# Kernel tuning notes

Hardware: AMD Instinct MI355X
Metric: run time of the kernel (lower is better)

The kernel has to match this reference:

```python
import jax, jax.numpy as jnp
import numpy as np

VNUMS = [4248, 4258, 5327, 3721, 5404, 2818]
B, C, H, W = 12, 64, 192, 192
DV, HID, BOX = 128, 256, 32


def _roi_patches(imgs, pros, imgbatch, box_len=BOX):
    # torchvision roi_align (aligned=False, sampling_ratio -> 1 sample per 1x1 bin):
    # bilinear sample at bin centers x1 + (j+0.5), y1 + (i+0.5)
    ar = jnp.arange(box_len, dtype=pros.dtype) + 0.5
    xs = pros[:, 0:1] - box_len / 2.0 + ar  # [G, box]
    ys = pros[:, 1:2] - box_len / 2.0 + ar  # [G, box]
    img_g = imgs[imgbatch]  # [G, C, H, W]

    def sample_one(img_chw, ys1, xs1):
        yy, xx = jnp.meshgrid(ys1, xs1, indexing="ij")  # [box, box]
        def per_c(ch):
            return jax.scipy.ndimage.map_coordinates(ch, [yy, xx], order=1, mode="nearest")
        return jax.vmap(per_c)(img_chw)  # [C, box, box]

    return jax.vmap(sample_one)(img_g, ys, xs)  # [G, C, box, box]


def setup_inputs() -> dict:
    key = jax.random.key(0)
    ks = jax.random.split(key, 6)
    G = 2 * B
    gtypes = np.array([(g // 2) % 6 if g % 2 == 0 else ((g // 2) + 3) % 6 for g in range(G)], dtype=np.int64)
    vnums_g = np.array([VNUMS[t] for t in gtypes])
    off = np.concatenate([[0], np.cumsum(vnums_g)])
    Nv = int(off[-1])  # 103104
    gar_of_vert = np.repeat(np.arange(G), vnums_g)
    idxs = []
    for t in range(6):
        gl = np.nonzero(gtypes == t)[0]
        idxs.append(np.concatenate([off[g] + np.arange(VNUMS[t]) for g in gl]).astype(np.int32))
    Din = DV + C
    pros = jax.random.uniform(ks[1], (G, 2), jnp.float32) * (H - 2.0 * BOX) + BOX
    inp = {
        "imgs": jax.random.normal(ks[0], (B, C, H, W), jnp.float32),
        "pros": pros,
        "x_verts": jax.random.normal(ks[2], (Nv, DV), jnp.float32),
        "W1": jax.random.normal(ks[3], (6, Din, HID), jnp.float32) / np.sqrt(Din).astype(np.float32),
        "W2": jax.random.normal(ks[4], (6, HID, HID), jnp.float32) / np.sqrt(HID).astype(np.float32),
        "W3": jax.random.normal(ks[5], (6, HID, 3), jnp.float32) / np.sqrt(HID).astype(np.float32),
        "imgbatch": jnp.asarray(np.arange(G) // 2, jnp.int32),
        "gar_of_vert": jnp.asarray(gar_of_vert, jnp.int32),
    }
    for t in range(6):
        inp[f"idx_t{t}"] = jnp.asarray(idxs[t])
    return inp


def reference(imgs, pros, x_verts, W1, W2, W3, imgbatch, gar_of_vert,
              idx_t0, idx_t1, idx_t2, idx_t3, idx_t4, idx_t5):
    # 1) roi_align patch extraction + pooled per-garment image feature
    patches = _roi_patches(imgs, pros, imgbatch)        # [G, C, 32, 32]
    garf = patches.mean(axis=(2, 3))                     # [G, C]
    # 2) per-vertex feature = [vertex feat | garment image feat]
    feat = jnp.concatenate([x_verts, garf[gar_of_vert]], axis=-1)  # [Nv, DV+C]
    # 3) MoE-style dispatch per garment type -> per-type expert MLP -> scatter-combine
    out = jnp.zeros((x_verts.shape[0], 3), feat.dtype)
    for t, idx in enumerate([idx_t0, idx_t1, idx_t2, idx_t3, idx_t4, idx_t5]):
        ft = feat[idx]                                   # gather (dispatch)
        h = jax.nn.relu(ft @ W1[t])
        h = jax.nn.relu(h @ W2[t])
        out = out.at[idx].set(h @ W3[t])                 # scatter (combine)
    return out
```

## Files before the change

kernel.cpp:

```cpp
#include <hip/hip_runtime.h>

typedef __attribute__((ext_vector_type(8))) short short8;
typedef __attribute__((ext_vector_type(4))) float float4_;

__device__ __forceinline__ unsigned short f2bf(float f) {
    unsigned u = __float_as_uint(f);
    u += 0x7FFFu + ((u >> 16) & 1u);
    return (unsigned short)(u >> 16);
}

__global__ void prep_weights(const float* __restrict__ W1,
                             const float* __restrict__ W2,
                             const float* __restrict__ W3,
                             unsigned short* __restrict__ w1t,
                             unsigned short* __restrict__ w2t,
                             unsigned short* __restrict__ w3t) {
    int id = blockIdx.x * 256 + threadIdx.x;
    if (id < 294912) {
        int t = id / 49152, r = id % 49152;
        int n = r / 192, k = r % 192;
        w1t[id] = f2bf(W1[(size_t)t * 49152 + k * 256 + n]);
    } else if (id < 688128) {
        int i2 = id - 294912;
        int t = i2 / 65536, r = i2 % 65536;
        int n = r / 256, k = r % 256;
        w2t[i2] = f2bf(W2[(size_t)t * 65536 + k * 256 + n]);
    } else if (id < 712704) {
        int i3 = id - 688128;
        int t = i3 / 4096, r = i3 % 4096;
        int n = r / 256, k = r % 256;
        w3t[i3] = (n < 3) ? f2bf(W3[(size_t)t * 768 + k * 3 + n]) : (unsigned short)0;
    }
}

__global__ void garf_kernel(const float* __restrict__ imgs,
                            const float* __restrict__ pros,
                            const int* __restrict__ imgbatch,
                            float* __restrict__ garf) {
    int g = blockIdx.x >> 3;
    int cblk = blockIdx.x & 7;
    int c = cblk * 8 + (threadIdx.x >> 5);
    int j = threadIdx.x & 31;
    int b = imgbatch[g];
    float cx = pros[g * 2 + 0], cy = pros[g * 2 + 1];

    float x = cx - 16.0f + (float)j + 0.5f;
    float xf = floorf(x);
    float wx1 = x - xf, wx0 = 1.0f - wx1;
    int ix0 = (int)xf, ix1 = ix0 + 1;
    ix0 = min(max(ix0, 0), 191); ix1 = min(max(ix1, 0), 191);

    const float* base = imgs + (size_t)(b * 64 + c) * (192 * 192);
    float sum = 0.0f;
    for (int i = 0; i < 32; ++i) {
        float y = cy - 16.0f + (float)i + 0.5f;
        float yf = floorf(y);
        float wy1 = y - yf, wy0 = 1.0f - wy1;
        int iy0 = (int)yf, iy1 = iy0 + 1;
        iy0 = min(max(iy0, 0), 191); iy1 = min(max(iy1, 0), 191);
        const float* r0 = base + iy0 * 192;
        const float* r1 = base + iy1 * 192;
        sum += wy0 * (wx0 * r0[ix0] + wx1 * r0[ix1]) +
               wy1 * (wx0 * r1[ix0] + wx1 * r1[ix1]);
    }
    for (int s = 16; s >= 1; s >>= 1) sum += __shfl_xor(sum, s);
    if (j == 0) garf[g * 64 + c] = sum * (1.0f / 1024.0f);
}

struct MoEArgs {
    const float* x_verts;
    const int* gar;
    const int* idx[6];
    const unsigned short* w1t;
    const unsigned short* w2t;
    const unsigned short* w3t;
    const float* garf;
    float* out;
    int cnt[6];
    int tile_end[6];
};

__global__ __launch_bounds__(256) void moe_kernel(MoEArgs a) {
    __shared__ __align__(16) char smem[24576 + 32768 + 512];
    char* sA = smem;
    char* sH = smem + 24576;
    float* sO = (float*)smem;
    int* sidx = (int*)(smem + 24576 + 32768);
    int* sg = sidx + 64;

    const int tid = threadIdx.x;
    int bt = blockIdx.x;
    int t = 0;
    while (t < 5 && bt >= a.tile_end[t]) ++t;
    const int tile = bt - (t ? a.tile_end[t - 1] : 0);
    const int cnt = a.cnt[t];
    const int i0 = tile * 64;
    const int* idx = a.idx[t];

    if (tid < 64) {
        int m = i0 + tid;
        if (m > cnt - 1) m = cnt - 1;
        int vid = idx[m];
        sidx[tid] = vid;
        sg[tid] = a.gar[vid];
    }
    __syncthreads();

    for (int e = tid; e < 1536; e += 256) {
        int m = e / 24, u = e % 24;
        const float* src;
        if (u < 16) src = a.x_verts + (size_t)sidx[m] * 128 + u * 8;
        else        src = a.garf + sg[m] * 64 + (u - 16) * 8;
        float4 v0 = ((const float4*)src)[0];
        float4 v1 = ((const float4*)src)[1];
        short8 pk;
        pk[0] = f2bf(v0.x); pk[1] = f2bf(v0.y); pk[2] = f2bf(v0.z); pk[3] = f2bf(v0.w);
        pk[4] = f2bf(v1.x); pk[5] = f2bf(v1.y); pk[6] = f2bf(v1.z); pk[7] = f2bf(v1.w);
        *(short8*)(sA + m * 384 + ((u ^ (m & 7)) * 16)) = pk;
    }
    __syncthreads();

    const int lane = tid & 63, w = tid >> 6, q = lane >> 4, l = lane & 15;

    float4_ acc[4][4] = {};
    const unsigned short* w1 = a.w1t + (size_t)t * 49152;
    for (int ks = 0; ks < 6; ++ks) {
        short8 af[4], bfr[4];
        for (int mt = 0; mt < 4; ++mt) {
            int row = mt * 16 + l;
            af[mt] = *(const short8*)(sA + row * 384 + (((ks * 4 + q) ^ (row & 7)) * 16));
        }
        for (int nt = 0; nt < 4; ++nt) {
            int n = w * 64 + nt * 16 + l;
            bfr[nt] = *(const short8*)(w1 + n * 192 + ks * 32 + q * 8);
        }
        for (int mt = 0; mt < 4; ++mt)
            for (int nt = 0; nt < 4; ++nt)
                acc[mt][nt] = __builtin_amdgcn_mfma_f32_16x16x32_bf16(
                    af[mt], bfr[nt], acc[mt][nt], 0, 0, 0);
    }
    for (int mt = 0; mt < 4; ++mt)
        for (int nt = 0; nt < 4; ++nt) {
            int n = w * 64 + nt * 16 + l;
            for (int r = 0; r < 4; ++r) {
                int m = mt * 16 + q * 4 + r;
                unsigned short b = f2bf(fmaxf(acc[mt][nt][r], 0.0f));
                *(unsigned short*)(sH + m * 512 + (((n >> 3) ^ (m & 7)) * 16) + (n & 7) * 2) = b;
            }
        }
    __syncthreads();

    float4_ acc2[4][4] = {};
    const unsigned short* w2 = a.w2t + (size_t)t * 65536;
    for (int ks = 0; ks < 8; ++ks) {
        short8 af[4], bfr[4];
        for (int mt = 0; mt < 4; ++mt) {
            int row = mt * 16 + l;
            af[mt] = *(const short8*)(sH + row * 512 + (((ks * 4 + q) ^ (row & 7)) * 16));
        }
        for (int nt = 0; nt < 4; ++nt) {
            int n = w * 64 + nt * 16 + l;
            bfr[nt] = *(const short8*)(w2 + n * 256 + ks * 32 + q * 8);
        }
        for (int mt = 0; mt < 4; ++mt)
            for (int nt = 0; nt < 4; ++nt)
                acc2[mt][nt] = __builtin_amdgcn_mfma_f32_16x16x32_bf16(
                    af[mt], bfr[nt], acc2[mt][nt], 0, 0, 0);
    }
    __syncthreads();
    for (int mt = 0; mt < 4; ++mt)
        for (int nt = 0; nt < 4; ++nt) {
            int n = w * 64 + nt * 16 + l;
            for (int r = 0; r < 4; ++r) {
                int m = mt * 16 + q * 4 + r;
                unsigned short b = f2bf(fmaxf(acc2[mt][nt][r], 0.0f));
                *(unsigned short*)(sH + m * 512 + (((n >> 3) ^ (m & 7)) * 16) + (n & 7) * 2) = b;
            }
        }
    __syncthreads();

    float4_ acc3[4] = {};
    const unsigned short* w3 = a.w3t + (size_t)t * 4096;
    for (int s2 = 0; s2 < 2; ++s2) {
        int ks = w * 2 + s2;
        short8 bf3 = *(const short8*)(w3 + l * 256 + ks * 32 + q * 8);
        for (int mt = 0; mt < 4; ++mt) {
            int row = mt * 16 + l;
            short8 af = *(const short8*)(sH + row * 512 + (((ks * 4 + q) ^ (row & 7)) * 16));
            acc3[mt] = __builtin_amdgcn_mfma_f32_16x16x32_bf16(af, bf3, acc3[mt], 0, 0, 0);
        }
    }
    float* sOw = sO + w * 1024;
    for (int mt = 0; mt < 4; ++mt)
        for (int r = 0; r < 4; ++r) {
            int m = mt * 16 + q * 4 + r;
            sOw[m * 16 + l] = acc3[mt][r];
        }
    __syncthreads();

    if (tid < 192) {
        int m = tid / 3, j = tid - m * 3;
        if (i0 + m < cnt) {
            float s = sO[m * 16 + j] + sO[1024 + m * 16 + j] +
                      sO[2048 + m * 16 + j] + sO[3072 + m * 16 + j];
            a.out[(size_t)sidx[m] * 3 + j] = s;
        }
    }
}

extern "C" void kernel_launch(void* const* d_in, const int* in_sizes, int n_in,
                              void* d_out, int out_size, void* d_ws, size_t ws_size,
                              hipStream_t stream) {
    const float* imgs    = (const float*)d_in[0];
    const float* pros    = (const float*)d_in[1];
    const float* x_verts = (const float*)d_in[2];
    const float* W1      = (const float*)d_in[3];
    const float* W2      = (const float*)d_in[4];
    const float* W3      = (const float*)d_in[5];
    const int* imgbatch  = (const int*)d_in[6];
    const int* gar       = (const int*)d_in[7];

    unsigned short* w1t = (unsigned short*)d_ws;
    unsigned short* w2t = (unsigned short*)((char*)d_ws + 589824);
    unsigned short* w3t = (unsigned short*)((char*)d_ws + 1376256);
    float* garf         = (float*)((char*)d_ws + 1425408);

    prep_weights<<<2784, 256, 0, stream>>>(W1, W2, W3, w1t, w2t, w3t);
    garf_kernel<<<24 * 8, 256, 0, stream>>>(imgs, pros, imgbatch, garf);

    MoEArgs a;
    a.x_verts = x_verts;
    a.gar = gar;
    for (int t = 0; t < 6; ++t) a.idx[t] = (const int*)d_in[8 + t];
    a.w1t = w1t; a.w2t = w2t; a.w3t = w3t;
    a.garf = garf;
    a.out = (float*)d_out;
    int tiles = 0;
    for (int t = 0; t < 6; ++t) {
        a.cnt[t] = in_sizes[8 + t];
        tiles += (a.cnt[t] + 63) / 64;
        a.tile_end[t] = tiles;
    }
    moe_kernel<<<tiles, 256, 0, stream>>>(a);
}
```

Baseline: 276.5 us.

## Merge prep and garf kernels, transpose MoE GEMMs, shrink shared memory

Combines weight preparation and ROI pooling into a single launch, with garf now split into one block per (garment, channel) and the weight transpose reading coalesced and writing scattered. The MoE kernel is reorganised so the weights form the A operand and vertices the B operand. This lets the activation buffer be reused in place, shared memory shrinks to 33KB, and launch bounds ask for 4 blocks per CU. The final layer computes per-vertex outputs directly and drops the cross-wave reduction through shared memory, at the cost of an extra barrier and packed-store layout changes.

Result: faster. 265.3 us (-4.1%).

```diff
diff --git a/kernel.cpp b/kernel.cpp
--- a/kernel.cpp
+++ b/kernel.cpp
@@ -9,62 +9,68 @@
     return (unsigned short)(u >> 16);
 }
 
-__global__ void prep_weights(const float* __restrict__ W1,
-                             const float* __restrict__ W2,
-                             const float* __restrict__ W3,
-                             unsigned short* __restrict__ w1t,
-                             unsigned short* __restrict__ w2t,
-                             unsigned short* __restrict__ w3t) {
-    int id = blockIdx.x * 256 + threadIdx.x;
-    if (id < 294912) {
-        int t = id / 49152, r = id % 49152;
-        int n = r / 192, k = r % 192;
-        w1t[id] = f2bf(W1[(size_t)t * 49152 + k * 256 + n]);
-    } else if (id < 688128) {
-        int i2 = id - 294912;
-        int t = i2 / 65536, r = i2 % 65536;
-        int n = r / 256, k = r % 256;
-        w2t[i2] = f2bf(W2[(size_t)t * 65536 + k * 256 + n]);
-    } else if (id < 712704) {
-        int i3 = id - 688128;
-        int t = i3 / 4096, r = i3 % 4096;
-        int n = r / 256, k = r % 256;
-        w3t[i3] = (n < 3) ? f2bf(W3[(size_t)t * 768 + k * 3 + n]) : (unsigned short)0;
-    }
-}
-
-__global__ void garf_kernel(const float* __restrict__ imgs,
-                            const float* __restrict__ pros,
-                            const int* __restrict__ imgbatch,
-                            float* __restrict__ garf) {
-    int g = blockIdx.x >> 3;
-    int cblk = blockIdx.x & 7;
-    int c = cblk * 8 + (threadIdx.x >> 5);
-    int j = threadIdx.x & 31;
-    int b = imgbatch[g];
-    float cx = pros[g * 2 + 0], cy = pros[g * 2 + 1];
-
-    float x = cx - 16.0f + (float)j + 0.5f;
-    float xf = floorf(x);
-    float wx1 = x - xf, wx0 = 1.0f - wx1;
-    int ix0 = (int)xf, ix1 = ix0 + 1;
-    ix0 = min(max(ix0, 0), 191); ix1 = min(max(ix1, 0), 191);
-
-    const float* base = imgs + (size_t)(b * 64 + c) * (192 * 192);
-    float sum = 0.0f;
-    for (int i = 0; i < 32; ++i) {
+#define GARF_BLOCKS 1536
+#define PREP_BLOCKS 2784
+
+__global__ void prep_garf(const float* __restrict__ imgs,
+                          const float* __restrict__ pros,
+                          const int* __restrict__ imgbatch,
+                          const float* __restrict__ W1,
+                          const float* __restrict__ W2,
+                          const float* __restrict__ W3,
+                          unsigned short* __restrict__ w1t,
+                          unsigned short* __restrict__ w2t,
+                          unsigned short* __restrict__ w3t,
+                          float* __restrict__ garf) {
+    const int tid = threadIdx.x;
+    if (blockIdx.x < GARF_BLOCKS) {
+        __shared__ float part[4];
+        int pc = blockIdx.x;
+        int g = pc >> 6, c = pc & 63;
+        int b = imgbatch[g];
+        float cx = pros[g * 2 + 0], cy = pros[g * 2 + 1];
+        int i = tid >> 3;
+        int j0 = (tid & 7) * 4;
         float y = cy - 16.0f + (float)i + 0.5f;
         float yf = floorf(y);
         float wy1 = y - yf, wy0 = 1.0f - wy1;
-        int iy0 = (int)yf, iy1 = iy0 + 1;
-        iy0 = min(max(iy0, 0), 191); iy1 = min(max(iy1, 0), 191);
+        int iy0 = min(max((int)yf, 0), 191), iy1 = min(max((int)yf + 1, 0), 191);
+        const float* base = imgs + (size_t)(b * 64 + c) * 36864;
         const float* r0 = base + iy0 * 192;
         const float* r1 = base + iy1 * 192;
-        sum += wy0 * (wx0 * r0[ix0] + wx1 * r0[ix1]) +
-               wy1 * (wx0 * r1[ix0] + wx1 * r1[ix1]);
-    }
-    for (int s = 16; s >= 1; s >>= 1) sum += __shfl_xor(sum, s);
-    if (j == 0) garf[g * 64 + c] = sum * (1.0f / 1024.0f);
+        float sum = 0.0f;
+#pragma unroll
+        for (int jj = 0; jj < 4; ++jj) {
+            float x = cx - 16.0f + (float)(j0 + jj) + 0.5f;
+            float xf = floorf(x);
+            float wx1 = x - xf, wx0 = 1.0f - wx1;
+            int ix0 = min(max((int)xf, 0), 191), ix1 = min(max((int)xf + 1, 0), 191);
+            sum += wy0 * (wx0 * r0[ix0] + wx1 * r0[ix1]) +
+                   wy1 * (wx0 * r1[ix0] + wx1 * r1[ix1]);
+        }
+        for (int s = 32; s >= 1; s >>= 1) sum += __shfl_xor(sum, s);
+        if ((tid & 63) == 0) part[tid >> 6] = sum;
+        __syncthreads();
+        if (tid == 0)
+            garf[g * 64 + c] = (part[0] + part[1] + part[2] + part[3]) * (1.0f / 1024.0f);
+    } else {
+        int id = (blockIdx.x - GARF_BLOCKS) * 256 + tid;
+        if (id < 294912) {
+            int t = id / 49152, r = id % 49152;
+            int k = r >> 8, n = r & 255;
+            w1t[t * 49152 + n * 192 + k] = f2bf(W1[id]);
+        } else if (id < 688128) {
+            int i2 = id - 294912;
+            int t = i2 >> 16, r = i2 & 65535;
+            int k = r >> 8, n = r & 255;
+            w2t[t * 65536 + n * 256 + k] = f2bf(W2[i2]);
+        } else if (id < 712704) {
+            int i3 = id - 688128;
+            int t = i3 >> 12, r = i3 & 4095;
+            int n = r >> 8, k = r & 255;
+            w3t[i3] = (n < 3) ? f2bf(W3[t * 768 + k * 3 + n]) : (unsigned short)0;
+        }
+    }
 }
 
 struct MoEArgs {
@@ -80,12 +86,10 @@
     int tile_end[6];
 };
 
-__global__ __launch_bounds__(256) void moe_kernel(MoEArgs a) {
-    __shared__ __align__(16) char smem[24576 + 32768 + 512];
-    char* sA = smem;
-    char* sH = smem + 24576;
-    float* sO = (float*)smem;
-    int* sidx = (int*)(smem + 24576 + 32768);
+__global__ __launch_bounds__(256, 4) void moe_kernel(MoEArgs a) {
+    __shared__ __align__(16) char smem[32768 + 512];
+    char* sF = smem;
+    int* sidx = (int*)(smem + 32768);
     int* sg = sidx + 64;
 
     const int tid = threadIdx.x;
@@ -116,7 +120,7 @@
         short8 pk;
         pk[0] = f2bf(v0.x); pk[1] = f2bf(v0.y); pk[2] = f2bf(v0.z); pk[3] = f2bf(v0.w);
         pk[4] = f2bf(v1.x); pk[5] = f2bf(v1.y); pk[6] = f2bf(v1.z); pk[7] = f2bf(v1.w);
-        *(short8*)(sA + m * 384 + ((u ^ (m & 7)) * 16)) = pk;
+        *(short8*)(sF + m * 384 + ((u ^ (m & 7)) * 16)) = pk;
     }
     __syncthreads();
 
@@ -127,26 +131,31 @@
     for (int ks = 0; ks < 6; ++ks) {
         short8 af[4], bfr[4];
         for (int mt = 0; mt < 4; ++mt) {
-            int row = mt * 16 + l;
-            af[mt] = *(const short8*)(sA + row * 384 + (((ks * 4 + q) ^ (row & 7)) * 16));
-        }
-        for (int nt = 0; nt < 4; ++nt) {
-            int n = w * 64 + nt * 16 + l;
-            bfr[nt] = *(const short8*)(w1 + n * 192 + ks * 32 + q * 8);
+            int hid = w * 64 + mt * 16 + l;
+            af[mt] = *(const short8*)(w1 + hid * 192 + ks * 32 + q * 8);
+        }
+        for (int nt = 0; nt < 4; ++nt) {
+            int v = nt * 16 + l;
+            bfr[nt] = *(const short8*)(sF + v * 384 + (((ks * 4 + q) ^ (v & 7)) * 16));
         }
         for (int mt = 0; mt < 4; ++mt)
             for (int nt = 0; nt < 4; ++nt)
                 acc[mt][nt] = __builtin_amdgcn_mfma_f32_16x16x32_bf16(
                     af[mt], bfr[nt], acc[mt][nt], 0, 0, 0);
     }
+    __syncthreads();
+
     for (int mt = 0; mt < 4; ++mt)
         for (int nt = 0; nt < 4; ++nt) {
-            int n = w * 64 + nt * 16 + l;
-            for (int r = 0; r < 4; ++r) {
-                int m = mt * 16 + q * 4 + r;
-                unsigned short b = f2bf(fmaxf(acc[mt][nt][r], 0.0f));
-                *(unsigned short*)(sH + m * 512 + (((n >> 3) ^ (m & 7)) * 16) + (n & 7) * 2) = b;
-            }
+            int v = nt * 16 + l;
+            int hu8 = w * 16 + mt * 4 + q;
+            int ku16 = hu8 >> 1, par = hu8 & 1;
+            uint2 pk;
+            pk.x = (unsigned)f2bf(fmaxf(acc[mt][nt][0], 0.0f)) |
+                   ((unsigned)f2bf(fmaxf(acc[mt][nt][1], 0.0f)) << 16);
+            pk.y = (unsigned)f2bf(fmaxf(acc[mt][nt][2], 0.0f)) |
+                   ((unsigned)f2bf(fmaxf(acc[mt][nt][3], 0.0f)) << 16);
+            *(uint2*)(sF + v * 512 + ((ku16 ^ (v & 7)) * 16) + par * 8) = pk;
         }
     __syncthreads();
 
@@ -155,12 +164,12 @@
     for (int ks = 0; ks < 8; ++ks) {
         short8 af[4], bfr[4];
         for (int mt = 0; mt < 4; ++mt) {
-            int row = mt * 16 + l;
-            af[mt] = *(const short8*)(sH + row * 512 + (((ks * 4 + q) ^ (row & 7)) * 16));
-        }
-        for (int nt = 0; nt < 4; ++nt) {
-            int n = w * 64 + nt * 16 + l;
-            bfr[nt] = *(const short8*)(w2 + n * 256 + ks * 32 + q * 8);
+            int hid = w * 64 + mt * 16 + l;
+            af[mt] = *(const short8*)(w2 + hid * 256 + ks * 32 + q * 8);
+        }
+        for (int nt = 0; nt < 4; ++nt) {
+            int v = nt * 16 + l;
+            bfr[nt] = *(const short8*)(sF + v * 512 + (((ks * 4 + q) ^ (v & 7)) * 16));
         }
         for (int mt = 0; mt < 4; ++mt)
             for (int nt = 0; nt < 4; ++nt)
@@ -168,42 +177,34 @@
                     af[mt], bfr[nt], acc2[mt][nt], 0, 0, 0);
     }
     __syncthreads();
+
     for (int mt = 0; mt < 4; ++mt)
         for (int nt = 0; nt < 4; ++nt) {
-            int n = w * 64 + nt * 16 + l;
-            for (int r = 0; r < 4; ++r) {
-                int m = mt * 16 + q * 4 + r;
-                unsigned short b = f2bf(fmaxf(acc2[mt][nt][r], 0.0f));
-                *(unsigned short*)(sH + m * 512 + (((n >> 3) ^ (m & 7)) * 16) + (n & 7) * 2) = b;
-            }
-        }
-    __syncthreads();
-
-    float4_ acc3[4] = {};
+            int v = nt * 16 + l;
+            int hu8 = w * 16 + mt * 4 + q;
+            int ku16 = hu8 >> 1, par = hu8 & 1;
+            uint2 pk;
+            pk.x = (unsigned)f2bf(fmaxf(acc2[mt][nt][0], 0.0f)) |
+                   ((unsigned)f2bf(fmaxf(acc2[mt][nt][1], 0.0f)) << 16);
+            pk.y = (unsigned)f2bf(fmaxf(acc2[mt][nt][2], 0.0f)) |
+                   ((unsigned)f2bf(fmaxf(acc2[mt][nt][3], 0.0f)) << 16);
+            *(uint2*)(sF + v * 512 + ((ku16 ^ (v & 7)) * 16) + par * 8) = pk;
+        }
+    __syncthreads();
+
+    float4_ acc3 = {};
     const unsigned short* w3 = a.w3t + (size_t)t * 4096;
-    for (int s2 = 0; s2 < 2; ++s2) {
-        int ks = w * 2 + s2;
-        short8 bf3 = *(const short8*)(w3 + l * 256 + ks * 32 + q * 8);
-        for (int mt = 0; mt < 4; ++mt) {
-            int row = mt * 16 + l;
-            short8 af = *(const short8*)(sH + row * 512 + (((ks * 4 + q) ^ (row & 7)) * 16));
-            acc3[mt] = __builtin_amdgcn_mfma_f32_16x16x32_bf16(af, bf3, acc3[mt], 0, 0, 0);
-        }
-    }
-    float* sOw = sO + w * 1024;
-    for (int mt = 0; mt < 4; ++mt)
-        for (int r = 0; r < 4; ++r) {
-            int m = mt * 16 + q * 4 + r;
-            sOw[m * 16 + l] = acc3[mt][r];
-        }
-    __syncthreads();
-
-    if (tid < 192) {
-        int m = tid / 3, j = tid - m * 3;
-        if (i0 + m < cnt) {
-            float s = sO[m * 16 + j] + sO[1024 + m * 16 + j] +
-                      sO[2048 + m * 16 + j] + sO[3072 + m * 16 + j];
-            a.out[(size_t)sidx[m] * 3 + j] = s;
+    int v3 = w * 16 + l;
+    for (int ks = 0; ks < 8; ++ks) {
+        short8 a3 = *(const short8*)(w3 + l * 256 + ks * 32 + q * 8);
+        short8 b3 = *(const short8*)(sF + v3 * 512 + (((ks * 4 + q) ^ (v3 & 7)) * 16));
+        acc3 = __builtin_amdgcn_mfma_f32_16x16x32_bf16(a3, b3, acc3, 0, 0, 0);
+    }
+    if (q == 0) {
+        int m = i0 + v3;
+        if (m < cnt) {
+            float* o = a.out + (size_t)sidx[v3] * 3;
+            o[0] = acc3[0]; o[1] = acc3[1]; o[2] = acc3[2];
         }
     }
 }
@@ -225,8 +226,8 @@
     unsigned short* w3t = (unsigned short*)((char*)d_ws + 1376256);
     float* garf         = (float*)((char*)d_ws + 1425408);
 
-    prep_weights<<<2784, 256, 0, stream>>>(W1, W2, W3, w1t, w2t, w3t);
-    garf_kernel<<<24 * 8, 256, 0, stream>>>(imgs, pros, imgbatch, garf);
+    prep_garf<<<GARF_BLOCKS + PREP_BLOCKS, 256, 0, stream>>>(
+        imgs, pros, imgbatch, W1, W2, W3, w1t, w2t, w3t, garf);
 
     MoEArgs a;
     a.x_verts = x_verts;
```
